# Optimization experiments

Hardware: AMD Instinct MI355X
Metric: run time of the kernel (lower is better)

Reference implementation:

```python
import jax, jax.numpy as jnp
import numpy as np

B, S, D, H = 4, 2048, 1024, 16
HD = D // H

def setup_inputs() -> dict:
    key = jax.random.key(0)
    ks = jax.random.split(key, 11)
    s = 1.0 / np.sqrt(D)
    def lin(k):
        kw, kb = jax.random.split(k)
        return (jax.random.uniform(kw, (D, D), jnp.float32, -s, s),
                jax.random.uniform(kb, (D,), jnp.float32, -s, s))
    Wq, bq = lin(ks[0]); Wk, bk = lin(ks[1]); Wv, bv = lin(ks[2]); Wo, bo = lin(ks[3])
    return {
        "query": jax.random.normal(ks[4], (B, S, D), jnp.float32),
        "key": jax.random.normal(ks[5], (B, S, D), jnp.float32),
        "value": jax.random.normal(ks[6], (B, S, D), jnp.float32),
        "Wq": Wq, "bq": bq, "Wk": Wk, "bk": bk,
        "Wv": Wv, "bv": bv, "Wo": Wo, "bo": bo,
    }

def reference(query, key, value, Wq, bq, Wk, bk, Wv, bv, Wo, bo):
    def split_heads(x):  # [B,S,D] -> [B,H,S,HD]
        return x.reshape(B, S, H, HD).transpose(0, 2, 1, 3)
    q = split_heads(query @ Wq + bq)
    k = split_heads(key @ Wk + bk)
    v = split_heads(value @ Wv + bv)
    scores = jnp.einsum('bhqd,bhkd->bhqk', q, k) / np.sqrt(HD)
    probs = jax.nn.softmax(scores, axis=-1)
    ctx = jnp.einsum('bhqk,bhkd->bhqd', probs, v)
    ctx = ctx.transpose(0, 2, 1, 3).reshape(B, S, D)
    return ctx @ Wo + bo
```

## Files before the change

kernel.cpp:

```cpp
#include <hip/hip_runtime.h>
#include <hip/hip_bf16.h>

#define B_ 4
#define S_ 2048
#define D_ 1024
#define H_ 16
#define HD_ 64
#define M_ (B_*S_)

typedef __bf16 bf16;
typedef bf16 bf16x8 __attribute__((ext_vector_type(8)));
typedef bf16 bf16x4 __attribute__((ext_vector_type(4)));
typedef float f32x4 __attribute__((ext_vector_type(4)));

__device__ __forceinline__ void gload_lds16(const void* g, void* l) {
  __builtin_amdgcn_global_load_lds((const __attribute__((address_space(1))) void*)g,
                                   (__attribute__((address_space(3))) void*)l, 16, 0, 0);
}

__global__ __launch_bounds__(256)
void wtrans_kernel(const float* __restrict__ Wq, const float* __restrict__ Wk,
                   const float* __restrict__ Wv, const float* __restrict__ Wo,
                   bf16* __restrict__ Wqt, bf16* __restrict__ Wkt,
                   bf16* __restrict__ Wvt, bf16* __restrict__ Wot) {
  __shared__ float tile[64][65];
  const float* W; bf16* Wt;
  switch (blockIdx.z) {
    case 0: W = Wq; Wt = Wqt; break;
    case 1: W = Wk; Wt = Wkt; break;
    case 2: W = Wv; Wt = Wvt; break;
    default: W = Wo; Wt = Wot; break;
  }
  int n0 = blockIdx.x * 64, k0 = blockIdx.y * 64;
  int tx = threadIdx.x & 63, ty = threadIdx.x >> 6;
#pragma unroll
  for (int i = 0; i < 16; i++) {
    int k = ty + i * 4;
    tile[k][tx] = W[(size_t)(k0 + k) * D_ + n0 + tx];
  }
  __syncthreads();
#pragma unroll
  for (int i = 0; i < 16; i++) {
    int n = ty + i * 4;
    Wt[(size_t)(n0 + n) * D_ + k0 + tx] = (bf16)tile[tx][n];
  }
}

#define BK 32
#define LDA 40
#define QSCALE 0.18033688011112042f

__global__ __launch_bounds__(256)
void proj_gemm_kernel(const float* __restrict__ Aq, const float* __restrict__ Ak,
                      const float* __restrict__ Av,
                      const bf16* __restrict__ Wqt, const bf16* __restrict__ Wkt,
                      const bf16* __restrict__ Wvt,
                      const float* __restrict__ bq, const float* __restrict__ bk,
                      const float* __restrict__ bv,
                      bf16* __restrict__ qb, bf16* __restrict__ kb, bf16* __restrict__ vbT) {
  __shared__ bf16 As[128 * LDA];
  __shared__ bf16 Bs[128 * LDA];
  const float* A; const bf16* Bt; const float* bias; float scale;
  if (blockIdx.z == 0)      { A = Aq; Bt = Wqt; bias = bq; scale = QSCALE; }
  else if (blockIdx.z == 1) { A = Ak; Bt = Wkt; bias = bk; scale = 1.0f; }
  else                      { A = Av; Bt = Wvt; bias = bv; scale = 1.0f; }

  const int n0 = blockIdx.x * 128, m0 = blockIdx.y * 128;
  const int tid = threadIdx.x;
  const int lane = tid & 63, w = tid >> 6;
  const int wr = w >> 1, wc = w & 1;
  const int l15 = lane & 15, quad = lane >> 4;

  f32x4 acc[4][4] = {};

  for (int kt = 0; kt < D_ / BK; kt++) {
    const int k0 = kt * BK;
#pragma unroll
    for (int i = 0; i < 4; i++) {
      int f = tid + i * 256;
      int row = f >> 3, cc = f & 7;
      const float4 v = *(const float4*)(A + (size_t)(m0 + row) * D_ + k0 + cc * 4);
      bf16x4 hv; hv[0] = (bf16)v.x; hv[1] = (bf16)v.y; hv[2] = (bf16)v.z; hv[3] = (bf16)v.w;
      *(bf16x4*)(&As[row * LDA + cc * 4]) = hv;
    }
#pragma unroll
    for (int i = 0; i < 2; i++) {
      int c = tid + i * 256;
      int row = c >> 2, cc = c & 3;
      bf16x8 v = *(const bf16x8*)(Bt + (size_t)(n0 + row) * D_ + k0 + cc * 8);
      *(bf16x8*)(&Bs[row * LDA + cc * 8]) = v;
    }
    __syncthreads();

    bf16x8 a[4], b[4];
#pragma unroll
    for (int fm = 0; fm < 4; fm++)
      a[fm] = *(const bf16x8*)(&As[(wr * 64 + fm * 16 + l15) * LDA + quad * 8]);
#pragma unroll
    for (int fn = 0; fn < 4; fn++)
      b[fn] = *(const bf16x8*)(&Bs[(wc * 64 + fn * 16 + l15) * LDA + quad * 8]);
#pragma unroll
    for (int fm = 0; fm < 4; fm++)
#pragma unroll
      for (int fn = 0; fn < 4; fn++)
        acc[fm][fn] = __builtin_amdgcn_mfma_f32_16x16x32_bf16(a[fm], b[fn], acc[fm][fn], 0, 0, 0);
    __syncthreads();
  }
  if (blockIdx.z < 2) {
    bf16* C = (blockIdx.z == 0) ? qb : kb;
#pragma unroll
    for (int fm = 0; fm < 4; fm++) {
      int row = m0 + wr * 64 + fm * 16 + quad * 4;
#pragma unroll
      for (int fn = 0; fn < 4; fn++) {
        int col = n0 + wc * 64 + fn * 16 + l15;
        float bval = bias[col];
#pragma unroll
        for (int r = 0; r < 4; r++)
          C[(size_t)(row + r) * D_ + col] = (bf16)((acc[fm][fn][r] + bval) * scale);
      }
    }
  } else {
#pragma unroll
    for (int fm = 0; fm < 4; fm++) {
      int row = m0 + wr * 64 + fm * 16 + quad * 4;
#pragma unroll
      for (int fn = 0; fn < 4; fn++) {
        int col = n0 + wc * 64 + fn * 16 + l15;
        float bval = bias[col];
        bf16x4 pk;
#pragma unroll
        for (int r = 0; r < 4; r++) pk[r] = (bf16)(acc[fm][fn][r] + bval);
        *(bf16x4*)(vbT + (size_t)col * M_ + row) = pk;
      }
    }
  }
}

#define LPS 72

__global__ __launch_bounds__(256)
void attn_kernel(const bf16* __restrict__ qb, const bf16* __restrict__ kb,
                 const bf16* __restrict__ vbT, bf16* __restrict__ ctxb) {
  __shared__ bf16 Ks[2][64 * 64];
  __shared__ bf16 Vs[2][64 * 64];
  __shared__ bf16 Ps[128 * LPS];

  const int bh = blockIdx.y;
  const int b = bh >> 4, h = bh & 15;
  const int q0 = blockIdx.x * 128;
  const int tid = threadIdx.x, lane = tid & 63, w = tid >> 6;
  const int l15 = lane & 15, quad = lane >> 4;

  const size_t baseQ = ((size_t)(b * S_ + q0)) * D_ + h * HD_;

  bf16x8 qf[2][2];
#pragma unroll
  for (int fm = 0; fm < 2; fm++)
#pragma unroll
    for (int ks = 0; ks < 2; ks++)
      qf[fm][ks] = *(const bf16x8*)(qb + baseQ + (size_t)(w * 32 + fm * 16 + l15) * D_ + ks * 32 + quad * 8);

  f32x4 o[2][4] = {};
  float li[2][4] = {};

  const int srow_i = lane >> 3;
  const int schunk = lane & 7;

  auto stage = [&](int buf, int kt) {
#pragma unroll
    for (int t = 0; t < 2; t++) {
      const int r0 = w * 16 + t * 8;
      const int row = r0 + srow_i;
      const int c = schunk ^ (row & 7);
      const bf16* gK = kb + ((size_t)(b * S_ + kt * 64 + row)) * D_ + h * 64 + c * 8;
      gload_lds16(gK, &Ks[buf][r0 * 64]);
      const bf16* gV = vbT + ((size_t)(h * 64 + row)) * M_ + b * S_ + kt * 64 + c * 8;
      gload_lds16(gV, &Vs[buf][r0 * 64]);
    }
  };

  stage(0, 0);
  __syncthreads();

  for (int kt = 0; kt < S_ / 64; kt++) {
    const int buf = kt & 1;
    if (kt + 1 < S_ / 64) stage(buf ^ 1, kt + 1);

    f32x4 s[2][4] = {};
#pragma unroll
    for (int ks = 0; ks < 2; ks++) {
#pragma unroll
      for (int fn = 0; fn < 4; fn++) {
        const int key = fn * 16 + l15;
        bf16x8 kf = *(const bf16x8*)(&Ks[buf][key * 64 + (((ks * 4 + quad) ^ (key & 7)) * 8)]);
#pragma unroll
        for (int fm = 0; fm < 2; fm++)
          s[fm][fn] = __builtin_amdgcn_mfma_f32_16x16x32_bf16(qf[fm][ks], kf, s[fm][fn], 0, 0, 0);
      }
    }

#pragma unroll
    for (int fm = 0; fm < 2; fm++) {
#pragma unroll
      for (int r = 0; r < 4; r++) {
        const int prow = (w * 32 + fm * 16 + quad * 4 + r) * LPS;
        float rs = 0.f;
#pragma unroll
        for (int fn = 0; fn < 4; fn++) {
          float p = __builtin_amdgcn_exp2f(s[fm][fn][r]);
          rs += p;
          Ps[prow + fn * 16 + l15] = (bf16)p;
        }
        li[fm][r] += rs;
      }
    }

#pragma unroll
    for (int ks2 = 0; ks2 < 2; ks2++) {
      bf16x8 pf[2], vf[4];
#pragma unroll
      for (int fm = 0; fm < 2; fm++)
        pf[fm] = *(const bf16x8*)(&Ps[(w * 32 + fm * 16 + l15) * LPS + ks2 * 32 + quad * 8]);
#pragma unroll
      for (int fd = 0; fd < 4; fd++) {
        const int d = fd * 16 + l15;
        vf[fd] = *(const bf16x8*)(&Vs[buf][d * 64 + (((ks2 * 4 + quad) ^ (d & 7)) * 8)]);
      }
#pragma unroll
      for (int fm = 0; fm < 2; fm++)
#pragma unroll
        for (int fd = 0; fd < 4; fd++)
          o[fm][fd] = __builtin_amdgcn_mfma_f32_16x16x32_bf16(pf[fm], vf[fd], o[fm][fd], 0, 0, 0);
    }
    __syncthreads();
  }

#pragma unroll
  for (int fm = 0; fm < 2; fm++) {
#pragma unroll
    for (int r = 0; r < 4; r++) {
      float l = li[fm][r];
      l += __shfl_xor(l, 1);
      l += __shfl_xor(l, 2);
      l += __shfl_xor(l, 4);
      l += __shfl_xor(l, 8);
      float inv = 1.0f / l;
      int row = w * 32 + fm * 16 + quad * 4 + r;
#pragma unroll
      for (int fd = 0; fd < 4; fd++)
        ctxb[baseQ + (size_t)row * D_ + fd * 16 + l15] = (bf16)(o[fm][fd][r] * inv);
    }
  }
}

__global__ __launch_bounds__(256)
void out_gemm_kernel(const bf16* __restrict__ A, const bf16* __restrict__ Bt,
                     const float* __restrict__ bias, float* __restrict__ Cout) {
  __shared__ bf16 As[128 * LDA];
  __shared__ bf16 Bs[128 * LDA];
  const int n0 = blockIdx.x * 128, m0 = blockIdx.y * 128;
  const int tid = threadIdx.x;
  const int lane = tid & 63, w = tid >> 6;
  const int wr = w >> 1, wc = w & 1;
  const int l15 = lane & 15, quad = lane >> 4;

  f32x4 acc[4][4] = {};

  for (int kt = 0; kt < D_ / BK; kt++) {
    const int k0 = kt * BK;
#pragma unroll
    for (int i = 0; i < 2; i++) {
      int c = tid + i * 256;
      int row = c >> 2, cc = c & 3;
      bf16x8 v = *(const bf16x8*)(A + (size_t)(m0 + row) * D_ + k0 + cc * 8);
      *(bf16x8*)(&As[row * LDA + cc * 8]) = v;
    }
#pragma unroll
    for (int i = 0; i < 2; i++) {
      int c = tid + i * 256;
      int row = c >> 2, cc = c & 3;
      bf16x8 v = *(const bf16x8*)(Bt + (size_t)(n0 + row) * D_ + k0 + cc * 8);
      *(bf16x8*)(&Bs[row * LDA + cc * 8]) = v;
    }
    __syncthreads();

    bf16x8 a[4], b[4];
#pragma unroll
    for (int fm = 0; fm < 4; fm++)
      a[fm] = *(const bf16x8*)(&As[(wr * 64 + fm * 16 + l15) * LDA + quad * 8]);
#pragma unroll
    for (int fn = 0; fn < 4; fn++)
      b[fn] = *(const bf16x8*)(&Bs[(wc * 64 + fn * 16 + l15) * LDA + quad * 8]);
#pragma unroll
    for (int fm = 0; fm < 4; fm++)
#pragma unroll
      for (int fn = 0; fn < 4; fn++)
        acc[fm][fn] = __builtin_amdgcn_mfma_f32_16x16x32_bf16(a[fm], b[fn], acc[fm][fn], 0, 0, 0);
    __syncthreads();
  }
#pragma unroll
  for (int fm = 0; fm < 4; fm++) {
    int row = m0 + wr * 64 + fm * 16 + quad * 4;
#pragma unroll
    for (int fn = 0; fn < 4; fn++) {
      int col = n0 + wc * 64 + fn * 16 + l15;
      float bval = bias[col];
#pragma unroll
      for (int r = 0; r < 4; r++)
        Cout[(size_t)(row + r) * D_ + col] = acc[fm][fn][r] + bval;
    }
  }
}

extern "C" void kernel_launch(void* const* d_in, const int* in_sizes, int n_in,
                              void* d_out, int out_size, void* d_ws, size_t ws_size,
                              hipStream_t stream) {
  const float* query = (const float*)d_in[0];
  const float* key   = (const float*)d_in[1];
  const float* value = (const float*)d_in[2];
  const float* Wq = (const float*)d_in[3];
  const float* bq = (const float*)d_in[4];
  const float* Wk = (const float*)d_in[5];
  const float* bk = (const float*)d_in[6];
  const float* Wv = (const float*)d_in[7];
  const float* bv = (const float*)d_in[8];
  const float* Wo = (const float*)d_in[9];
  const float* bo = (const float*)d_in[10];
  float* out = (float*)d_out;

  char* ws = (char*)d_ws;
  const size_t WT_BYTES = (size_t)D_ * D_ * sizeof(bf16);
  const size_t MD_BYTES = (size_t)M_ * D_ * sizeof(bf16);
  bf16* Wqt  = (bf16*)(ws);
  bf16* Wkt  = (bf16*)(ws + WT_BYTES);
  bf16* Wvt  = (bf16*)(ws + 2 * WT_BYTES);
  bf16* Wot  = (bf16*)(ws + 3 * WT_BYTES);
  bf16* qb   = (bf16*)(ws + 4 * WT_BYTES);
  bf16* kb   = (bf16*)(ws + 4 * WT_BYTES + MD_BYTES);
  bf16* vbT  = (bf16*)(ws + 4 * WT_BYTES + 2 * MD_BYTES);
  bf16* ctxb = (bf16*)(ws + 4 * WT_BYTES + 3 * MD_BYTES);

  wtrans_kernel<<<dim3(D_ / 64, D_ / 64, 4), 256, 0, stream>>>(
      Wq, Wk, Wv, Wo, Wqt, Wkt, Wvt, Wot);

  proj_gemm_kernel<<<dim3(D_ / 128, M_ / 128, 3), 256, 0, stream>>>(
      query, key, value, Wqt, Wkt, Wvt, bq, bk, bv, qb, kb, vbT);

  attn_kernel<<<dim3(S_ / 128, B_ * H_), 256, 0, stream>>>(qb, kb, vbT, ctxb);

  out_gemm_kernel<<<dim3(D_ / 128, M_ / 128), 256, 0, stream>>>(ctxb, Wot, bo, out);
}
```

Before: 414.5 us.

## Use direct-to-LDS loads with XOR swizzle in GEMMs and transpose QK^T in attention

Both GEMM kernels now use global_load_lds directly into XOR-swizzled LDS tiles with BK raised to 64. The projection GEMM stages fp32 activations in LDS and converts them to bf16 at fragment-load time, which removes the register round-trip and halves the number of loop iterations and barriers. The attention kernel computes S^T (K as the A operand) so each lane holds 4 consecutive keys. This allows packed bf16x4 stores of P and a per-lane row-sum instead of a 4-step shuffle reduction per row. The cost is more LDS (fp32 A tile of 32KB) and loads that are not double-buffered, so each tile load still stalls at the barrier.

```diff
diff --git a/kernel.cpp b/kernel.cpp
--- a/kernel.cpp
+++ b/kernel.cpp
@@ -46,8 +46,6 @@
   }
 }
 
-#define BK 32
-#define LDA 40
 #define QSCALE 0.18033688011112042f
 
 __global__ __launch_bounds__(256)
@@ -58,56 +56,72 @@
                       const float* __restrict__ bq, const float* __restrict__ bk,
                       const float* __restrict__ bv,
                       bf16* __restrict__ qb, bf16* __restrict__ kb, bf16* __restrict__ vbT) {
-  __shared__ bf16 As[128 * LDA];
-  __shared__ bf16 Bs[128 * LDA];
-  const float* A; const bf16* Bt; const float* bias; float scale;
-  if (blockIdx.z == 0)      { A = Aq; Bt = Wqt; bias = bq; scale = QSCALE; }
-  else if (blockIdx.z == 1) { A = Ak; Bt = Wkt; bias = bk; scale = 1.0f; }
-  else                      { A = Av; Bt = Wvt; bias = bv; scale = 1.0f; }
+  __shared__ float Asf[128 * 64];
+  __shared__ bf16  Bs[128 * 64];
+  const float* A; const bf16* Bt; const float* bias;
+  if (blockIdx.z == 0)      { A = Aq; Bt = Wqt; bias = bq; }
+  else if (blockIdx.z == 1) { A = Ak; Bt = Wkt; bias = bk; }
+  else                      { A = Av; Bt = Wvt; bias = bv; }
 
   const int n0 = blockIdx.x * 128, m0 = blockIdx.y * 128;
   const int tid = threadIdx.x;
   const int lane = tid & 63, w = tid >> 6;
   const int wr = w >> 1, wc = w & 1;
   const int l15 = lane & 15, quad = lane >> 4;
+  const int arow_sub = lane >> 4, achk = lane & 15;
+  const int brow_sub = lane >> 3, bchk = lane & 7;
 
   f32x4 acc[4][4] = {};
 
-  for (int kt = 0; kt < D_ / BK; kt++) {
-    const int k0 = kt * BK;
-#pragma unroll
-    for (int i = 0; i < 4; i++) {
-      int f = tid + i * 256;
-      int row = f >> 3, cc = f & 7;
-      const float4 v = *(const float4*)(A + (size_t)(m0 + row) * D_ + k0 + cc * 4);
-      bf16x4 hv; hv[0] = (bf16)v.x; hv[1] = (bf16)v.y; hv[2] = (bf16)v.z; hv[3] = (bf16)v.w;
-      *(bf16x4*)(&As[row * LDA + cc * 4]) = hv;
-    }
-#pragma unroll
-    for (int i = 0; i < 2; i++) {
-      int c = tid + i * 256;
-      int row = c >> 2, cc = c & 3;
-      bf16x8 v = *(const bf16x8*)(Bt + (size_t)(n0 + row) * D_ + k0 + cc * 8);
-      *(bf16x8*)(&Bs[row * LDA + cc * 8]) = v;
-    }
-    __syncthreads();
-
-    bf16x8 a[4], b[4];
-#pragma unroll
-    for (int fm = 0; fm < 4; fm++)
-      a[fm] = *(const bf16x8*)(&As[(wr * 64 + fm * 16 + l15) * LDA + quad * 8]);
-#pragma unroll
-    for (int fn = 0; fn < 4; fn++)
-      b[fn] = *(const bf16x8*)(&Bs[(wc * 64 + fn * 16 + l15) * LDA + quad * 8]);
-#pragma unroll
-    for (int fm = 0; fm < 4; fm++)
-#pragma unroll
-      for (int fn = 0; fn < 4; fn++)
-        acc[fm][fn] = __builtin_amdgcn_mfma_f32_16x16x32_bf16(a[fm], b[fn], acc[fm][fn], 0, 0, 0);
-    __syncthreads();
-  }
+  for (int kt = 0; kt < D_ / 64; kt++) {
+    const int k0 = kt * 64;
+#pragma unroll
+    for (int t = 0; t < 8; t++) {
+      int r0 = w * 32 + t * 4;
+      int row = r0 + arow_sub;
+      int cg = achk ^ (row & 15);
+      gload_lds16(A + (size_t)(m0 + row) * D_ + k0 + cg * 4, &Asf[r0 * 64]);
+    }
+#pragma unroll
+    for (int t = 0; t < 4; t++) {
+      int r0 = w * 32 + t * 8;
+      int row = r0 + brow_sub;
+      int cg = bchk ^ (row & 7);
+      gload_lds16(Bt + (size_t)(n0 + row) * D_ + k0 + cg * 8, &Bs[r0 * 64]);
+    }
+    __syncthreads();
+
+#pragma unroll
+    for (int ks = 0; ks < 2; ks++) {
+      bf16x8 a[4], b[4];
+#pragma unroll
+      for (int fm = 0; fm < 4; fm++) {
+        int row = wr * 64 + fm * 16 + l15;
+        int cl = (ks * 8 + quad * 2) ^ (row & 15);
+        f32x4 lo = *(const f32x4*)(&Asf[row * 64 + cl * 4]);
+        f32x4 hi = *(const f32x4*)(&Asf[row * 64 + (cl ^ 1) * 4]);
+        bf16x8 av;
+        av[0] = (bf16)lo[0]; av[1] = (bf16)lo[1]; av[2] = (bf16)lo[2]; av[3] = (bf16)lo[3];
+        av[4] = (bf16)hi[0]; av[5] = (bf16)hi[1]; av[6] = (bf16)hi[2]; av[7] = (bf16)hi[3];
+        a[fm] = av;
+      }
+#pragma unroll
+      for (int fn = 0; fn < 4; fn++) {
+        int row = wc * 64 + fn * 16 + l15;
+        b[fn] = *(const bf16x8*)(&Bs[row * 64 + (((ks * 4 + quad) ^ (row & 7)) * 8)]);
+      }
+#pragma unroll
+      for (int fm = 0; fm < 4; fm++)
+#pragma unroll
+        for (int fn = 0; fn < 4; fn++)
+          acc[fm][fn] = __builtin_amdgcn_mfma_f32_16x16x32_bf16(a[fm], b[fn], acc[fm][fn], 0, 0, 0);
+    }
+    __syncthreads();
+  }
+
   if (blockIdx.z < 2) {
     bf16* C = (blockIdx.z == 0) ? qb : kb;
+    float scale = (blockIdx.z == 0) ? QSCALE : 1.0f;
 #pragma unroll
     for (int fm = 0; fm < 4; fm++) {
       int row = m0 + wr * 64 + fm * 16 + quad * 4;
@@ -145,6 +159,7 @@
   __shared__ bf16 Ks[2][64 * 64];
   __shared__ bf16 Vs[2][64 * 64];
   __shared__ bf16 Ps[128 * LPS];
+  __shared__ float Lf[128];
 
   const int bh = blockIdx.y;
   const int b = bh >> 4, h = bh & 15;
@@ -162,7 +177,7 @@
       qf[fm][ks] = *(const bf16x8*)(qb + baseQ + (size_t)(w * 32 + fm * 16 + l15) * D_ + ks * 32 + quad * 8);
 
   f32x4 o[2][4] = {};
-  float li[2][4] = {};
+  float li[2] = {0.f, 0.f};
 
   const int srow_i = lane >> 3;
   const int schunk = lane & 7;
@@ -187,32 +202,32 @@
     const int buf = kt & 1;
     if (kt + 1 < S_ / 64) stage(buf ^ 1, kt + 1);
 
-    f32x4 s[2][4] = {};
+    f32x4 st[4][2] = {};
 #pragma unroll
     for (int ks = 0; ks < 2; ks++) {
 #pragma unroll
-      for (int fn = 0; fn < 4; fn++) {
-        const int key = fn * 16 + l15;
+      for (int fk = 0; fk < 4; fk++) {
+        const int key = fk * 16 + l15;
         bf16x8 kf = *(const bf16x8*)(&Ks[buf][key * 64 + (((ks * 4 + quad) ^ (key & 7)) * 8)]);
 #pragma unroll
-        for (int fm = 0; fm < 2; fm++)
-          s[fm][fn] = __builtin_amdgcn_mfma_f32_16x16x32_bf16(qf[fm][ks], kf, s[fm][fn], 0, 0, 0);
-      }
-    }
-
-#pragma unroll
-    for (int fm = 0; fm < 2; fm++) {
-#pragma unroll
-      for (int r = 0; r < 4; r++) {
-        const int prow = (w * 32 + fm * 16 + quad * 4 + r) * LPS;
-        float rs = 0.f;
-#pragma unroll
-        for (int fn = 0; fn < 4; fn++) {
-          float p = __builtin_amdgcn_exp2f(s[fm][fn][r]);
-          rs += p;
-          Ps[prow + fn * 16 + l15] = (bf16)p;
-        }
-        li[fm][r] += rs;
+        for (int fq = 0; fq < 2; fq++)
+          st[fk][fq] = __builtin_amdgcn_mfma_f32_16x16x32_bf16(kf, qf[fq][ks], st[fk][fq], 0, 0, 0);
+      }
+    }
+
+#pragma unroll
+    for (int fq = 0; fq < 2; fq++) {
+      const int prow = (w * 32 + fq * 16 + l15) * LPS;
+#pragma unroll
+      for (int fk = 0; fk < 4; fk++) {
+        float p0 = __builtin_amdgcn_exp2f(st[fk][fq][0]);
+        float p1 = __builtin_amdgcn_exp2f(st[fk][fq][1]);
+        float p2 = __builtin_amdgcn_exp2f(st[fk][fq][2]);
+        float p3 = __builtin_amdgcn_exp2f(st[fk][fq][3]);
+        li[fq] += (p0 + p1) + (p2 + p3);
+        bf16x4 pk;
+        pk[0] = (bf16)p0; pk[1] = (bf16)p1; pk[2] = (bf16)p2; pk[3] = (bf16)p3;
+        *(bf16x4*)(&Ps[prow + fk * 16 + quad * 4]) = pk;
       }
     }
 
@@ -237,15 +252,18 @@
   }
 
 #pragma unroll
+  for (int fq = 0; fq < 2; fq++) {
+    float l = li[fq];
+    l += __shfl_xor(l, 16);
+    l += __shfl_xor(l, 32);
+    if (quad == 0) Lf[w * 32 + fq * 16 + l15] = l;
+  }
+#pragma unroll
   for (int fm = 0; fm < 2; fm++) {
+    f32x4 l4 = *(const f32x4*)(&Lf[w * 32 + fm * 16 + quad * 4]);
 #pragma unroll
     for (int r = 0; r < 4; r++) {
-      float l = li[fm][r];
-      l += __shfl_xor(l, 1);
-      l += __shfl_xor(l, 2);
-      l += __shfl_xor(l, 4);
-      l += __shfl_xor(l, 8);
-      float inv = 1.0f / l;
+      float inv = 1.0f / l4[r];
       int row = w * 32 + fm * 16 + quad * 4 + r;
 #pragma unroll
       for (int fd = 0; fd < 4; fd++)
@@ -257,46 +275,48 @@
 __global__ __launch_bounds__(256)
 void out_gemm_kernel(const bf16* __restrict__ A, const bf16* __restrict__ Bt,
                      const float* __restrict__ bias, float* __restrict__ Cout) {
-  __shared__ bf16 As[128 * LDA];
-  __shared__ bf16 Bs[128 * LDA];
+  __shared__ bf16 As[128 * 64];
+  __shared__ bf16 Bs[128 * 64];
   const int n0 = blockIdx.x * 128, m0 = blockIdx.y * 128;
   const int tid = threadIdx.x;
   const int lane = tid & 63, w = tid >> 6;
   const int wr = w >> 1, wc = w & 1;
   const int l15 = lane & 15, quad = lane >> 4;
+  const int srow = lane >> 3, schunk = lane & 7;
 
   f32x4 acc[4][4] = {};
 
-  for (int kt = 0; kt < D_ / BK; kt++) {
-    const int k0 = kt * BK;
-#pragma unroll
-    for (int i = 0; i < 2; i++) {
-      int c = tid + i * 256;
-      int row = c >> 2, cc = c & 3;
-      bf16x8 v = *(const bf16x8*)(A + (size_t)(m0 + row) * D_ + k0 + cc * 8);
-      *(bf16x8*)(&As[row * LDA + cc * 8]) = v;
-    }
-#pragma unroll
-    for (int i = 0; i < 2; i++) {
-      int c = tid + i * 256;
-      int row = c >> 2, cc = c & 3;
-      bf16x8 v = *(const bf16x8*)(Bt + (size_t)(n0 + row) * D_ + k0 + cc * 8);
-      *(bf16x8*)(&Bs[row * LDA + cc * 8]) = v;
-    }
-    __syncthreads();
-
-    bf16x8 a[4], b[4];
-#pragma unroll
-    for (int fm = 0; fm < 4; fm++)
-      a[fm] = *(const bf16x8*)(&As[(wr * 64 + fm * 16 + l15) * LDA + quad * 8]);
-#pragma unroll
-    for (int fn = 0; fn < 4; fn++)
-      b[fn] = *(const bf16x8*)(&Bs[(wc * 64 + fn * 16 + l15) * LDA + quad * 8]);
-#pragma unroll
-    for (int fm = 0; fm < 4; fm++)
-#pragma unroll
-      for (int fn = 0; fn < 4; fn++)
-        acc[fm][fn] = __builtin_amdgcn_mfma_f32_16x16x32_bf16(a[fm], b[fn], acc[fm][fn], 0, 0, 0);
+  for (int kt = 0; kt < D_ / 64; kt++) {
+    const int k0 = kt * 64;
+#pragma unroll
+    for (int t = 0; t < 4; t++) {
+      int r0 = w * 32 + t * 8;
+      int row = r0 + srow;
+      int cg = schunk ^ (row & 7);
+      gload_lds16(A + (size_t)(m0 + row) * D_ + k0 + cg * 8, &As[r0 * 64]);
+      gload_lds16(Bt + (size_t)(n0 + row) * D_ + k0 + cg * 8, &Bs[r0 * 64]);
+    }
+    __syncthreads();
+
+#pragma unroll
+    for (int ks = 0; ks < 2; ks++) {
+      bf16x8 a[4], b[4];
+#pragma unroll
+      for (int fm = 0; fm < 4; fm++) {
+        int row = wr * 64 + fm * 16 + l15;
+        a[fm] = *(const bf16x8*)(&As[row * 64 + (((ks * 4 + quad) ^ (row & 7)) * 8)]);
+      }
+#pragma unroll
+      for (int fn = 0; fn < 4; fn++) {
+        int row = wc * 64 + fn * 16 + l15;
+        b[fn] = *(const bf16x8*)(&Bs[row * 64 + (((ks * 4 + quad) ^ (row & 7)) * 8)]);
+      }
+#pragma unroll
+      for (int fm = 0; fm < 4; fm++)
+#pragma unroll
+        for (int fn = 0; fn < 4; fn++)
+          acc[fm][fn] = __builtin_amdgcn_mfma_f32_16x16x32_bf16(a[fm], b[fn], acc[fm][fn], 0, 0, 0);
+    }
     __syncthreads();
   }
 #pragma unroll
```

Measured after the change: 379.0 us. 8.6% less time.
